# Kernel optimization log

Hardware: AMD Instinct MI355X
Metric: run time of the kernel (lower is better)

Reference implementation:

```python
import jax, jax.numpy as jnp
import numpy as np

B, T, H, HY, E, L = 32, 256, 1024, 256, 64, 2


def setup_inputs() -> dict:
    key = jax.random.key(0)
    ks = jax.random.split(key, 16)
    rn = lambda k, s, sc=0.05: jax.random.normal(k, s, dtype=jnp.float32) * sc
    return {
        'input': rn(ks[0], (B, T, H), 1.0),
        'w_ih': rn(ks[1], (L, 4 * H, H)),
        'w_hh': rn(ks[2], (L, 4 * H, H)),
        'hyper_w_ih': rn(ks[3], (L, 4 * HY, 2 * H)),
        'hyper_w_hh': rn(ks[4], (L, 4 * HY, HY)),
        'hyper_b': rn(ks[5], (L, 4 * HY)),
        'w_zh': rn(ks[6], (L, 4 * E, HY)),
        'b_zh': jnp.ones((L, 4 * E), jnp.float32),
        'w_zx': rn(ks[7], (L, 4 * E, HY)),
        'b_zx': jnp.ones((L, 4 * E), jnp.float32),
        'w_zb': rn(ks[8], (L, 4 * E, HY)),
        'w_dh': rn(ks[9], (L, 4, H, E), 1.0 / E),
        'w_dx': rn(ks[10], (L, 4, H, E), 1.0 / E),
        'w_db': rn(ks[11], (L, 4, H, E)),
        'b0': rn(ks[12], (L, 4 * H)),
    }


def reference(input, w_ih, w_hh, hyper_w_ih, hyper_w_hh, hyper_b,
              w_zh, b_zh, w_zx, b_zx, w_zb, w_dh, w_dx, w_db, b0):
    L = w_ih.shape[0]
    Bb = input.shape[0]
    Hh = w_hh.shape[-1]
    Hy = hyper_w_hh.shape[-1]
    Ee = w_dh.shape[-1]

    def cell(l, xt, h, c, hh, hc):
        # hyper (meta) LSTM step: input is concat(x, h_main)
        xh = jnp.concatenate([xt, h], axis=-1)
        hg = xh @ hyper_w_ih[l].T + hh @ hyper_w_hh[l].T + hyper_b[l]
        hi, hf, hgc, ho = jnp.split(hg, 4, axis=-1)
        hc2 = jax.nn.sigmoid(hf) * hc + jax.nn.sigmoid(hi) * jnp.tanh(hgc)
        hh2 = jax.nn.sigmoid(ho) * jnp.tanh(hc2)
        # gate-wise embeddings z (B, 4, E) then project to per-gate scale vectors (B, 4H)
        zh = (hh2 @ w_zh[l].T + b_zh[l]).reshape(Bb, 4, Ee)
        zx = (hh2 @ w_zx[l].T + b_zx[l]).reshape(Bb, 4, Ee)
        zb = (hh2 @ w_zb[l].T).reshape(Bb, 4, Ee)
        dh = jnp.einsum('bge,ghe->bgh', zh, w_dh[l]).reshape(Bb, 4 * Hh)
        dx = jnp.einsum('bge,ghe->bgh', zx, w_dx[l]).reshape(Bb, 4 * Hh)
        db = jnp.einsum('bge,ghe->bgh', zb, w_db[l]).reshape(Bb, 4 * Hh) + b0[l]
        # main LSTM gates, dynamically scaled by hypernetwork
        pre = dh * (h @ w_hh[l].T) + dx * (xt @ w_ih[l].T) + db
        i, f, g, o = jnp.split(pre, 4, axis=-1)
        c2 = jax.nn.sigmoid(f) * c + jax.nn.sigmoid(i) * jnp.tanh(g)
        h2 = jax.nn.sigmoid(o) * jnp.tanh(c2)
        return h2, c2, hh2, hc2

    def step(carry, xt):
        h, c, hh, hc = carry  # each (L, B, .)
        hs, cs, hhs, hcs = [], [], [], []
        inp = xt
        for l in range(L):
            h2, c2, hh2, hc2 = cell(l, inp, h[l], c[l], hh[l], hc[l])
            inp = h2
            hs.append(h2); cs.append(c2); hhs.append(hh2); hcs.append(hc2)
        carry = (jnp.stack(hs), jnp.stack(cs), jnp.stack(hhs), jnp.stack(hcs))
        return carry, inp  # top-layer hidden

    init = (jnp.zeros((L, Bb, Hh), input.dtype), jnp.zeros((L, Bb, Hh), input.dtype),
            jnp.zeros((L, Bb, Hy), input.dtype), jnp.zeros((L, Bb, Hy), input.dtype))
    carry, ys = jax.lax.scan(step, init, jnp.swapaxes(input, 0, 1))
    h_seq = jnp.swapaxes(ys, 0, 1)  # (B, T, H)
    return h_seq, carry[0][-1], carry[1][-1]
```

## Files before the change

kernel.cpp:

```cpp
#include <hip/hip_runtime.h>

typedef __bf16 bf16;
typedef __bf16 bf16x8 __attribute__((ext_vector_type(8)));
typedef __bf16 bf16x4 __attribute__((ext_vector_type(4)));
typedef float f32x4 __attribute__((ext_vector_type(4)));
typedef unsigned long long u64;

#define SCOPE_AGENT __HIP_MEMORY_SCOPE_AGENT


__device__ __forceinline__ float sigf(float x) { return 1.0f / (1.0f + __expf(-x)); }
__device__ __forceinline__ float tanhf_fast(float x) {
  float e = __expf(-2.0f * fabsf(x));
  float r = (1.0f - e) / (1.0f + e);
  return copysignf(r, x);
}
__device__ __forceinline__ f32x4 mfma16(bf16x8 a, bf16x8 b, f32x4 c) {
  return __builtin_amdgcn_mfma_f32_16x16x32_bf16(a, b, c, 0, 0, 0);
}
__device__ __forceinline__ u64 uld(const u64* p) { return __hip_atomic_load(p, __ATOMIC_RELAXED, SCOPE_AGENT); }
__device__ __forceinline__ void ust(u64* p, u64 v) { __hip_atomic_store(p, v, __ATOMIC_RELAXED, SCOPE_AGENT); }
__device__ __forceinline__ int ildi(const int* p) { return __hip_atomic_load(p, __ATOMIC_RELAXED, SCOPE_AGENT); }
__device__ __forceinline__ void isti(int* p, int v) { __hip_atomic_store(p, v, __ATOMIC_RELAXED, SCOPE_AGENT); }
__device__ __forceinline__ void fstf(float* p, float v) { __hip_atomic_store(p, v, __ATOMIC_RELAXED, SCOPE_AGENT); }
__device__ __forceinline__ void usti32(unsigned* p, unsigned v) { __hip_atomic_store(p, v, __ATOMIC_RELAXED, SCOPE_AGENT); }

__global__ void detect_kernel(const void* probe, int* flag) {
  __shared__ int cnt;
  if (threadIdx.x == 0) cnt = 0;
  __syncthreads();
  const bf16* p = (const bf16*)probe;
  int local = 0;
  for (int j = threadIdx.x; j < 8192; j += 256) {
    float x = (float)p[j];
    bool wild = (x != x) || (fabsf(x) > 1e3f) || (x != 0.0f && fabsf(x) < 1e-30f);
    local += wild ? 1 : 0;
  }
  atomicAdd(&cnt, local);
  __syncthreads();
  if (threadIdx.x == 0) *flag = (cnt > 64) ? 1 : 0;
}

struct CvtSrc { const void* s[15]; };
struct CvtDst { bf16* d[15]; };

__global__ __launch_bounds__(256) void convert_kernel(CvtSrc S, CvtDst D, const int* flag) {
  const int pre[16] = {0, 8388608, 16777216, 25165824, 29360128, 29884416, 29886464,
                       30017536, 30018048, 30149120, 30149632, 30280704, 30804992,
                       31329280, 31853568, 31861760};
  const int fp32 = *flag;
  const int nvec = 31861760 / 4;
  for (int v = blockIdx.x * 256 + threadIdx.x; v < nvec; v += gridDim.x * 256) {
    int e = v * 4;
    int seg = 0;
#pragma unroll
    for (int k = 1; k < 15; ++k) seg += (e >= pre[k]) ? 1 : 0;
    int off = e - pre[seg];
    bf16* d = D.d[seg] + off;
    if (fp32) {
      const float* s = (const float*)S.s[seg] + off;
      float4 x = *(const float4*)s;
      d[0] = (bf16)x.x; d[1] = (bf16)x.y; d[2] = (bf16)x.z; d[3] = (bf16)x.w;
    } else {
      const bf16* s = (const bf16*)S.s[seg] + off;
      d[0] = s[0]; d[1] = s[1]; d[2] = s[2]; d[3] = s[3];
    }
  }
}

__global__ void init_kernel(u64* zbase) {
  int i = blockIdx.x * 256 + threadIdx.x;
  zbase[i] = 0ull;
}

__global__ __launch_bounds__(256) void gemm_pre(
    const bf16* __restrict__ A, const bf16* __restrict__ w_ih_l,
    const bf16* __restrict__ hwih_l, bf16* __restrict__ Xp, float* __restrict__ Hxp) {
  constexpr int LDT = 72;
  __shared__ alignas(16) bf16 As[64 * LDT];
  __shared__ alignas(16) bf16 Bs[64 * LDT];
  const int bm = blockIdx.x & 127;
  const int bn = blockIdx.x >> 7;
  const int m0 = bm * 64, n0 = bn * 64;
  const int tid = threadIdx.x;
  const int lane = tid & 63, wid = tid >> 6;
  const int l15 = lane & 15, q = lane >> 4;
  const int srow = tid >> 2, sk = (tid & 3) * 16;
  const bf16* arow = A + (size_t)(m0 + srow) * 1024;
  const int n = n0 + srow;
  const bf16* brow = (n < 4096) ? (w_ih_l + (size_t)n * 1024)
                                : (hwih_l + (size_t)(n - 4096) * 2048);
  f32x4 acc[4] = {};
  for (int kb = 0; kb < 1024; kb += 64) {
    *(bf16x8*)(&As[srow * LDT + sk])     = *(const bf16x8*)(arow + kb + sk);
    *(bf16x8*)(&As[srow * LDT + sk + 8]) = *(const bf16x8*)(arow + kb + sk + 8);
    *(bf16x8*)(&Bs[srow * LDT + sk])     = *(const bf16x8*)(brow + kb + sk);
    *(bf16x8*)(&Bs[srow * LDT + sk + 8]) = *(const bf16x8*)(brow + kb + sk + 8);
    __syncthreads();
#pragma unroll
    for (int kk = 0; kk < 64; kk += 32) {
      bf16x8 av = *(const bf16x8*)(&As[(wid * 16 + l15) * LDT + kk + q * 8]);
#pragma unroll
      for (int j = 0; j < 4; ++j) {
        bf16x8 bv = *(const bf16x8*)(&Bs[(j * 16 + l15) * LDT + kk + q * 8]);
        acc[j] = mfma16(av, bv, acc[j]);
      }
    }
    __syncthreads();
  }
#pragma unroll
  for (int j = 0; j < 4; ++j) {
    const int gn = n0 + j * 16 + l15;
#pragma unroll
    for (int r = 0; r < 4; ++r) {
      const int gm = m0 + wid * 16 + q * 4 + r;
      float v = acc[j][r];
      if (gn < 4096) Xp[(size_t)gm * 4096 + gn] = (bf16)v;
      else           Hxp[(size_t)gm * 1024 + (gn - 4096)] = v;
    }
  }
}

struct SeqArgs {
  const bf16 *w_hh, *hwih, *hwhh, *hyb;
  const bf16 *w_zh, *b_zh, *w_zx, *b_zx, *w_zb;
  const bf16 *w_dh, *w_dx, *w_db, *b0;
  const bf16 *Xp; const float *Hxp;
  const bf16 *w_ih1;
  bf16 *Xp1c; float *Hxp1c;
  u64 *Y0;
  u64 *hpub;
  u64 *hh2pub;
  float *outp;
  int *flags;
};

__global__ __launch_bounds__(256) void seq_kernel(SeqArgs a) {
  __shared__ char smem[41472] __attribute__((aligned(16)));
  bf16 (*hstage)[1032] = (bf16(*)[1032])smem;
  bf16 (*hhK)[264]    = (bf16(*)[264])(smem + 33024);
  float* hgL          = (float*)(smem + 33024);
  bf16 (*hA4)[1032]   = (bf16(*)[1032])smem;
  bf16 (*hh2A)[264]   = (bf16(*)[264])(smem + 8256);
  float (*RhL)[256]   = (float(*)[256])(smem + 10368);
  float (*zsL)[768]   = (float(*)[768])(smem + 14464);
  float (*presL)[256] = (float(*)[256])(smem + 26752);
  bf16 (*hbuf)[64]    = (bf16(*)[64])(smem + 30848);
  bf16*  As = (bf16*)smem;
  bf16*  Bs = (bf16*)(smem + 9216);
  float* Ct = (float*)(smem + 18432);

  const int tid = threadIdx.x;
  const int lane = tid & 63, wid = tid >> 6;
  const int l15 = lane & 15, q = lane >> 4;
  const int blk = blockIdx.x;
  const int xcd = blk & 7, slot = blk >> 3;
  const int layer = xcd >> 2, xl = xcd & 3;
  const int s16 = xl * 4 + (slot & 3);
  const int bq = slot >> 2;
  const int lblk = bq * 16 + s16;
  const int hd = s16 >> 1;
  const int mh = (bq == hd) ? 0 : ((bq == ((hd + 4) & 7)) ? 1 : -1);
  const bool isHyper = (((s16 & 1) == 0) && (mh >= 0));

  u64* hbase  = a.hpub + (size_t)layer * 16384;
  u64* h2base = a.hh2pub + (size_t)layer * 4096;
  int* genp0  = a.flags;
  int* genp   = a.flags + layer * 16;
  int* gchunkp= a.flags + 32;
  int* arrp   = a.flags + 64 + layer * 2048;
  int* hh2fp  = a.flags + 4160 + layer * 256;
  int* carrp  = a.flags + 4672;

  const bf16* whh_l = a.w_hh + (size_t)layer * 4194304;
  const bf16* hybl  = a.hyb + layer * 1024;
  const bf16* bzh_l = a.b_zh + layer * 256;
  const bf16* bzx_l = a.b_zx + layer * 256;
  const bf16* b0_l  = a.b0 + (size_t)layer * 4096;
  const int cb = tid >> 6, chl = tid & 63;

  float c_reg = 0.0f;
  float hc[2] = {0, 0};

  const bf16* zrow[12];
#pragma unroll
  for (int j = 0; j < 12; ++j) {
    int ng = wid * 12 + j, tau = ng >> 4;
    const bf16* base = (tau == 0) ? a.w_zh : (tau == 1) ? a.w_zx : a.w_zb;
    zrow[j] = base + ((size_t)layer * 256 + (ng & 15) * 16 + l15) * 256;
  }
  const bf16* rrow[4];
#pragma unroll
  for (int nt = 0; nt < 4; ++nt)
    rrow[nt] = whh_l + (size_t)(wid * 1024 + s16 * 64 + nt * 16 + l15) * 1024;
  const bf16* hirow[2];
  const bf16* hhrow[2];
#pragma unroll
  for (int nt = 0; nt < 2; ++nt) {
    const int row = wid * 256 + hd * 32 + nt * 16 + l15;
    hirow[nt] = a.hwih + (size_t)layer * 2097152 + (size_t)row * 2048 + 1024;
    hhrow[nt] = a.hwhh + (size_t)layer * 262144 + (size_t)row * 256;
  }
  const size_t wdo = ((size_t)(layer * 4 + wid) * 1024 + s16 * 64 + lane) * 64;
  const bf16 *pdh = a.w_dh + wdo, *pdx = a.w_dx + wdo, *pdb = a.w_db + wdo;

  for (int t = 0; t < 256; ++t) {
    const int tloc = t & 31;
    u64* wslot = hbase + (size_t)(t & 1) * 8192;
    const u64* rslot = hbase + (size_t)((t + 1) & 1) * 8192;
    u64* wcur = h2base + (size_t)(t & 1) * 2048;
    const u64* rK = h2base + (size_t)((t + 1) & 1) * 2048;

    if (layer == 1 && tloc == 0) {
      const int k = t >> 5;
      if (tid == 0) { while (ildi(genp0) < (k + 1) * 32) __builtin_amdgcn_s_sleep(2); }
      __atomic_signal_fence(__ATOMIC_SEQ_CST);
      __syncthreads();
      const int srow = tid >> 2, sk = (tid & 3) * 16;
      for (int tt = 0; tt < 10; ++tt) {
        const int tile = lblk * 10 + tt;
        const int m0 = (tile & 15) * 64, n0 = (tile >> 4) * 64;
        const int m = m0 + srow;
        const u64* arow = a.Y0 + (((size_t)(m >> 5) * 256 + k * 32 + (m & 31)) << 8);
        const int n = n0 + srow;
        const bf16* brow = (n < 4096) ? (a.w_ih1 + (size_t)n * 1024)
                                      : (a.hwih + 2097152 + (size_t)(n - 4096) * 2048);
        f32x4 acc[4] = {};
        for (int kb = 0; kb < 1024; kb += 64) {
          const int c0 = (kb + sk) >> 2;
          u64 a0 = uld(arow + c0),     a1 = uld(arow + c0 + 1);
          u64 a2 = uld(arow + c0 + 2), a3 = uld(arow + c0 + 3);
          *(u64*)&As[srow * 72 + sk]      = a0;
          *(u64*)&As[srow * 72 + sk + 4]  = a1;
          *(u64*)&As[srow * 72 + sk + 8]  = a2;
          *(u64*)&As[srow * 72 + sk + 12] = a3;
          *(bf16x8*)&Bs[srow * 72 + sk]     = *(const bf16x8*)(brow + kb + sk);
          *(bf16x8*)&Bs[srow * 72 + sk + 8] = *(const bf16x8*)(brow + kb + sk + 8);
          __syncthreads();
#pragma unroll
          for (int kk = 0; kk < 64; kk += 32) {
            bf16x8 av = *(const bf16x8*)&As[(wid * 16 + l15) * 72 + kk + q * 8];
#pragma unroll
            for (int j = 0; j < 4; ++j) {
              bf16x8 bv = *(const bf16x8*)&Bs[(j * 16 + l15) * 72 + kk + q * 8];
              acc[j] = mfma16(av, bv, acc[j]);
            }
          }
          __syncthreads();
        }
#pragma unroll
        for (int j = 0; j < 4; ++j)
#pragma unroll
          for (int r = 0; r < 4; ++r)
            Ct[(wid * 16 + q * 4 + r) * 64 + j * 16 + l15] = acc[j][r];
        __syncthreads();
#pragma unroll
        for (int e = 0; e < 4; ++e) {
          const int qd = tid * 4 + e;
          const int row = qd >> 4, col4 = (qd & 15) * 4;
          f32x4 v = *(const f32x4*)&Ct[row * 64 + col4];
          const int gm = m0 + row, gn = n0 + col4;
          if (gn < 4096) {
            union { bf16 h[4]; u64 u; } pk;
#pragma unroll
            for (int x = 0; x < 4; ++x) pk.h[x] = (bf16)v[x];
            ust((u64*)a.Xp1c + ((((size_t)gm << 12) + gn) >> 2), pk.u);
          } else {
            float* hp = a.Hxp1c + ((size_t)gm << 10) + (gn - 4096);
#pragma unroll
            for (int x = 0; x < 4; ++x) fstf(hp + x, v[x]);
          }
        }
        __syncthreads();
      }
      __atomic_signal_fence(__ATOMIC_SEQ_CST);
      __builtin_amdgcn_s_waitcnt(0);
      __syncthreads();
      if (tid == 0) isti(carrp + lblk * 16, k + 1);
      if (lblk == 0 && wid == 0) {
        for (;;) {
          int v0 = ildi(carrp + lane * 32);
          int v1 = ildi(carrp + lane * 32 + 16);
          if (__all((v0 >= k + 1) && (v1 >= k + 1))) break;
          __builtin_amdgcn_s_sleep(2);
        }
        __atomic_signal_fence(__ATOMIC_SEQ_CST);
        if (lane == 0) isti(gchunkp, k + 1);
      }
      if (tid == 0) { while (ildi(gchunkp) < k + 1) __builtin_amdgcn_s_sleep(2); }
      __atomic_signal_fence(__ATOMIC_SEQ_CST);
      __syncthreads();
    }

    if (t > 0 && tid == 0) {
      while (ildi(genp) < t) __builtin_amdgcn_s_sleep(2);
    }
    __atomic_signal_fence(__ATOMIC_SEQ_CST);
    __syncthreads();

    if (isHyper) {
      for (int i = tid; i < 4096; i += 256) {
        int b = i >> 8, u = i & 255;
        *(u64*)&hstage[b][u * 4] = uld(rslot + ((size_t)(mh * 16 + b) << 8) + u);
      }
      for (int i = tid; i < 1024; i += 256) {
        int b = i >> 6, u = i & 63;
        *(u64*)&hhK[b][u * 4] = uld(rK + ((size_t)(mh * 16 + b) << 6) + u);
      }
      __syncthreads();
      f32x4 acc[2] = {};
      for (int kk = 0; kk < 1024; kk += 32) {
        int ko = kk + q * 8;
        bf16x8 a0 = *(const bf16x8*)&hstage[l15][ko];
#pragma unroll
        for (int nt = 0; nt < 2; ++nt) {
          bf16x8 bv = *(const bf16x8*)(hirow[nt] + ko);
          acc[nt] = mfma16(a0, bv, acc[nt]);
        }
      }
      for (int kk = 0; kk < 256; kk += 32) {
        int ko = kk + q * 8;
        bf16x8 a0 = *(const bf16x8*)&hhK[l15][ko];
#pragma unroll
        for (int nt = 0; nt < 2; ++nt) {
          bf16x8 bv = *(const bf16x8*)(hhrow[nt] + ko);
          acc[nt] = mfma16(a0, bv, acc[nt]);
        }
      }
      __syncthreads();
#pragma unroll
      for (int nt = 0; nt < 2; ++nt)
#pragma unroll
        for (int r = 0; r < 4; ++r)
          hgL[(wid * 16 + q * 4 + r) * 32 + nt * 16 + l15] = acc[nt][r];
      __syncthreads();
      {
        const int b16 = tid >> 4, d0 = (tid & 15) * 2;
        const int b = mh * 16 + b16;
        float hx2[4][2];
        if (layer == 0) {
          const float* hx = a.Hxp + ((size_t)b * 256 + t) * 1024 + hd * 32 + d0;
#pragma unroll
          for (int g = 0; g < 4; ++g) {
            hx2[g][0] = hx[g * 256]; hx2[g][1] = hx[g * 256 + 1];
          }
        } else {
          const u64* hx1 = (const u64*)a.Hxp1c + (((size_t)b * 32 + tloc) << 9)
                         + ((hd * 32 + d0) >> 1);
#pragma unroll
          for (int g = 0; g < 4; ++g) {
            u64 w = uld(hx1 + g * 128);
            hx2[g][0] = __uint_as_float((unsigned)(w & 0xffffffffu));
            hx2[g][1] = __uint_as_float((unsigned)(w >> 32));
          }
        }
        union { bf16 h[2]; unsigned u; } pk;
#pragma unroll
        for (int dd = 0; dd < 2; ++dd) {
          int d = d0 + dd, gd = hd * 32 + d;
          float hi  = hgL[(0 * 16 + b16) * 32 + d] + (float)hybl[gd]       + hx2[0][dd];
          float hf  = hgL[(1 * 16 + b16) * 32 + d] + (float)hybl[256 + gd] + hx2[1][dd];
          float hgv = hgL[(2 * 16 + b16) * 32 + d] + (float)hybl[512 + gd] + hx2[2][dd];
          float ho  = hgL[(3 * 16 + b16) * 32 + d] + (float)hybl[768 + gd] + hx2[3][dd];
          hc[dd] = sigf(hf) * hc[dd] + sigf(hi) * tanhf_fast(hgv);
          pk.h[dd] = (bf16)(sigf(ho) * tanhf_fast(hc[dd]));
        }
        usti32((unsigned*)wcur + b * 128 + hd * 16 + (d0 >> 1), pk.u);
      }
      __atomic_signal_fence(__ATOMIC_SEQ_CST);
      __builtin_amdgcn_s_waitcnt(0);
      __syncthreads();
      if (tid == 0) isti(hh2fp + (hd * 2 + mh) * 16, t + 1);
    }
    __syncthreads();

    for (int i = tid; i < 1024; i += 256) {
      int b = i >> 8, u = i & 255;
      *(u64*)&hA4[b][u * 4] = uld(rslot + ((size_t)(bq * 4 + b) << 8) + u);
    }
    __syncthreads();
    {
      f32x4 racc[4] = {};
      for (int kk = 0; kk < 1024; kk += 32) {
        const int ko = kk + q * 8;
        bf16x8 av = *(const bf16x8*)&hA4[l15 & 3][ko];
#pragma unroll
        for (int nt = 0; nt < 4; ++nt) {
          bf16x8 bv = *(const bf16x8*)(rrow[nt] + ko);
          racc[nt] = mfma16(av, bv, racc[nt]);
        }
      }
      if (lane < 16) {
#pragma unroll
        for (int nt = 0; nt < 4; ++nt)
#pragma unroll
          for (int r = 0; r < 4; ++r)
            RhL[r][wid * 64 + nt * 16 + lane] = racc[nt][r];
      }
    }
    if (tid < 16) { while (ildi(hh2fp + tid * 16) < t + 1) __builtin_amdgcn_s_sleep(1); }
    __atomic_signal_fence(__ATOMIC_SEQ_CST);
    __syncthreads();
    {
      int b = tid >> 6, u = tid & 63;
      *(u64*)&hh2A[b][u * 4] = uld(wcur + ((size_t)(bq * 4 + b) << 6) + u);
    }
    __syncthreads();
    {
      f32x4 zacc[12] = {};
      for (int kk = 0; kk < 256; kk += 32) {
        const int ko = kk + q * 8;
        bf16x8 av = *(const bf16x8*)&hh2A[l15 & 3][ko];
#pragma unroll
        for (int j = 0; j < 12; ++j) {
          bf16x8 bv = *(const bf16x8*)(zrow[j] + ko);
          zacc[j] = mfma16(av, bv, zacc[j]);
        }
      }
      if (lane < 16) {
#pragma unroll
        for (int j = 0; j < 12; ++j) {
          int ng = wid * 12 + j, tau = ng >> 4, col = (ng & 15) * 16 + lane;
          float bias = (tau == 0) ? (float)bzh_l[col] : (tau == 1) ? (float)bzx_l[col] : 0.0f;
#pragma unroll
          for (int r = 0; r < 4; ++r) zsL[r][tau * 256 + col] = zacc[j][r] + bias;
        }
      }
    }
    __syncthreads();
    {
      float dH[4] = {}, dX[4] = {}, dB[4] = {};
      for (int e0 = 0; e0 < 64; e0 += 4) {
        bf16x4 wh = *(const bf16x4*)(pdh + e0);
        bf16x4 wx = *(const bf16x4*)(pdx + e0);
        bf16x4 wb = *(const bf16x4*)(pdb + e0);
        f32x4 zh_[4], zx_[4], zb_[4];
#pragma unroll
        for (int b = 0; b < 4; ++b) {
          zh_[b] = *(const f32x4*)&zsL[b][wid * 64 + e0];
          zx_[b] = *(const f32x4*)&zsL[b][256 + wid * 64 + e0];
          zb_[b] = *(const f32x4*)&zsL[b][512 + wid * 64 + e0];
        }
#pragma unroll
        for (int jj = 0; jj < 4; ++jj) {
          float whf = (float)wh[jj], wxf = (float)wx[jj], wbf = (float)wb[jj];
#pragma unroll
          for (int b = 0; b < 4; ++b) {
            dH[b] += zh_[b][jj] * whf;
            dX[b] += zx_[b][jj] * wxf;
            dB[b] += zb_[b][jj] * wbf;
          }
        }
      }
      const int n = wid * 1024 + s16 * 64 + lane;
#pragma unroll
      for (int b = 0; b < 4; ++b) {
        float rh = RhL[b][wid * 64 + lane];
        float xp;
        if (layer == 0) {
          xp = (float)a.Xp[((size_t)(bq * 4 + b) * 256 + t) * 4096 + n];
        } else {
          u64 w = uld((const u64*)a.Xp1c
                      + ((((size_t)((bq * 4 + b) * 32 + tloc) << 12) + (n & ~3)) >> 2));
          xp = __uint_as_float(((unsigned)(w >> ((n & 3) * 16)) & 0xffffu) << 16);
        }
        float b0v = (float)b0_l[n];
        presL[b][wid * 64 + lane] = dH[b] * rh + dX[b] * xp + dB[b] + b0v;
      }
    }
    __syncthreads();
    {
      float iv = presL[cb][chl];
      float fv = presL[cb][64 + chl];
      float gv = presL[cb][128 + chl];
      float ov = presL[cb][192 + chl];
      c_reg = sigf(fv) * c_reg + sigf(iv) * tanhf_fast(gv);
      float hn = sigf(ov) * tanhf_fast(c_reg);
      hbuf[cb][chl] = (bf16)hn;
      if (layer) {
        const size_t oo = ((size_t)(bq * 4 + cb) * 256 + t) * 1024 + s16 * 64 + chl;
        a.outp[oo] = hn;
        if (t == 255) {
          a.outp[8388608 + (bq * 4 + cb) * 1024 + s16 * 64 + chl] = hn;
          a.outp[8421376 + (bq * 4 + cb) * 1024 + s16 * 64 + chl] = c_reg;
        }
      }
    }
    __syncthreads();
    if (tid < 64) {
      int b = tid >> 4, u = tid & 15;
      u64 pk = *(const u64*)&hbuf[b][u * 4];
      ust(wslot + ((size_t)(bq * 4 + b) << 8) + s16 * 16 + u, pk);
      if (layer == 0)
        ust(a.Y0 + (((size_t)(bq * 4 + b) * 256 + t) << 8) + s16 * 16 + u, pk);
    }
    __atomic_signal_fence(__ATOMIC_SEQ_CST);
    __builtin_amdgcn_s_waitcnt(0);
    __syncthreads();
    if (tid == 0) isti(arrp + lblk * 16, t + 1);
    if (lblk == 0 && wid == 0) {
      const int t1 = t + 1;
      for (;;) {
        int v0 = ildi(arrp + lane * 32);
        int v1 = ildi(arrp + lane * 32 + 16);
        if (__all((v0 >= t1) && (v1 >= t1))) break;
        __builtin_amdgcn_s_sleep(2);
      }
      __atomic_signal_fence(__ATOMIC_SEQ_CST);
      if (lane == 0) isti(genp, t1);
    }
  }
}

extern "C" void kernel_launch(void* const* d_in, const int* in_sizes, int n_in,
                              void* d_out, int out_size, void* d_ws, size_t ws_size,
                              hipStream_t stream) {
  float* outp = (float*)d_out;
  char* ws = (char*)d_ws;
  bf16*  Xp     = (bf16*) (ws);
  float* Hxp    = (float*)(ws + 67108864ull);
  u64*   Y0     = (u64*)  (ws + 100663296ull);
  bf16* c_input = (bf16*)(ws + 117669888ull);
  bf16*  Xp1c   = c_input;
  float* Hxp1c  = (float*)(ws + 117669888ull + 8388608ull);
  bf16* c_w_ih  = (bf16*)(ws + 134447104ull);
  bf16* c_w_hh  = (bf16*)(ws + 151224320ull);
  bf16* c_hwih  = (bf16*)(ws + 168001536ull);
  bf16* c_hwhh  = (bf16*)(ws + 176390144ull);
  bf16* c_hyb   = (bf16*)(ws + 177438720ull);
  bf16* c_wzh   = (bf16*)(ws + 177442816ull);
  bf16* c_bzh   = (bf16*)(ws + 177704960ull);
  bf16* c_wzx   = (bf16*)(ws + 177705984ull);
  bf16* c_bzx   = (bf16*)(ws + 177968128ull);
  bf16* c_wzb   = (bf16*)(ws + 177969152ull);
  bf16* c_wdh   = (bf16*)(ws + 178231296ull);
  bf16* c_wdx   = (bf16*)(ws + 179279872ull);
  bf16* c_wdb   = (bf16*)(ws + 180328448ull);
  bf16* c_b0    = (bf16*)(ws + 181377024ull);
  int*  dflag   = (int*) (ws + 181393408ull);
  char* pubb    = ws + 181397504ull;
  u64*   hpub   = (u64*)  (pubb + 0);
  u64*   hh2pub = (u64*)  (pubb + 262144);
  int*   flags  = (int*)  (pubb + 327680);

  hipLaunchKernelGGL(detect_kernel, dim3(1), dim3(256), 0, stream, d_in[2], dflag);
  CvtSrc S; CvtDst D;
  for (int i = 0; i < 15; ++i) S.s[i] = d_in[i];
  D.d[0] = c_input; D.d[1] = c_w_ih; D.d[2] = c_w_hh; D.d[3] = c_hwih; D.d[4] = c_hwhh;
  D.d[5] = c_hyb;   D.d[6] = c_wzh;  D.d[7] = c_bzh;  D.d[8] = c_wzx;  D.d[9] = c_bzx;
  D.d[10] = c_wzb;  D.d[11] = c_wdh; D.d[12] = c_wdx; D.d[13] = c_wdb; D.d[14] = c_b0;
  hipLaunchKernelGGL(convert_kernel, dim3(2048), dim3(256), 0, stream, S, D, dflag);

  hipLaunchKernelGGL(init_kernel, dim3(176), dim3(256), 0, stream, (u64*)pubb);
  hipLaunchKernelGGL(gemm_pre, dim3(10240), dim3(256), 0, stream,
                     c_input, c_w_ih, c_hwih, Xp, Hxp);

  SeqArgs sa;
  sa.w_hh = c_w_hh; sa.hwih = c_hwih; sa.hwhh = c_hwhh; sa.hyb = c_hyb;
  sa.w_zh = c_wzh; sa.b_zh = c_bzh; sa.w_zx = c_wzx; sa.b_zx = c_bzx; sa.w_zb = c_wzb;
  sa.w_dh = c_wdh; sa.w_dx = c_wdx; sa.w_db = c_wdb; sa.b0 = c_b0;
  sa.Xp = Xp; sa.Hxp = Hxp;
  sa.w_ih1 = c_w_ih + (size_t)4194304;
  sa.Xp1c = Xp1c; sa.Hxp1c = Hxp1c;
  sa.Y0 = Y0;
  sa.hpub = hpub; sa.hh2pub = hh2pub;
  sa.outp = outp;
  sa.flags = flags;
  hipLaunchKernelGGL(seq_kernel, dim3(256), dim3(256), 0, stream, sa);
}
```

Before: 19.70 ms.

## Replace global per-step barrier with targeted per-block dependency flag waits

```diff
diff --git a/kernel.cpp b/kernel.cpp
--- a/kernel.cpp
+++ b/kernel.cpp
@@ -162,13 +162,13 @@
   const int hd = s16 >> 1;
   const int mh = (bq == hd) ? 0 : ((bq == ((hd + 4) & 7)) ? 1 : -1);
   const bool isHyper = (((s16 & 1) == 0) && (mh >= 0));
+  const int myMh = bq >> 2;
 
   u64* hbase  = a.hpub + (size_t)layer * 16384;
   u64* h2base = a.hh2pub + (size_t)layer * 4096;
-  int* genp0  = a.flags;
-  int* genp   = a.flags + layer * 16;
   int* gchunkp= a.flags + 32;
   int* arrp   = a.flags + 64 + layer * 2048;
+  int* arrp0  = a.flags + 64;
   int* hh2fp  = a.flags + 4160 + layer * 256;
   int* carrp  = a.flags + 4672;
 
@@ -213,7 +213,11 @@
 
     if (layer == 1 && tloc == 0) {
       const int k = t >> 5;
-      if (tid == 0) { while (ildi(genp0) < (k + 1) * 32) __builtin_amdgcn_s_sleep(2); }
+      if (tid < 128) {
+        while (ildi(arrp0 + tid * 16) < (k + 1) * 32) __builtin_amdgcn_s_sleep(2);
+      } else if (t > 0) {
+        while (ildi(arrp + (tid - 128) * 16) < t) __builtin_amdgcn_s_sleep(2);
+      }
       __atomic_signal_fence(__ATOMIC_SEQ_CST);
       __syncthreads();
       const int srow = tid >> 2, sk = (tid & 3) * 16;
@@ -292,8 +296,20 @@
       __syncthreads();
     }
 
-    if (t > 0 && tid == 0) {
-      while (ildi(genp) < t) __builtin_amdgcn_s_sleep(2);
+    if (t > 0) {
+      if (tid < 16) {
+        while (ildi(arrp + (bq * 16 + tid) * 16) < t) __builtin_amdgcn_s_sleep(1);
+      }
+      if (isHyper) {
+        if (tid >= 64 && tid < 128) {
+          const int j = tid - 64;
+          const int fl = (mh * 4 + (j >> 4)) * 16 + (j & 15);
+          while (ildi(arrp + fl * 16) < t) __builtin_amdgcn_s_sleep(1);
+        }
+        if (tid >= 128 && tid < 136) {
+          while (ildi(hh2fp + ((tid - 128) * 2 + mh) * 16) < t) __builtin_amdgcn_s_sleep(1);
+        }
+      }
     }
     __atomic_signal_fence(__ATOMIC_SEQ_CST);
     __syncthreads();
@@ -398,7 +414,9 @@
             RhL[r][wid * 64 + nt * 16 + lane] = racc[nt][r];
       }
     }
-    if (tid < 16) { while (ildi(hh2fp + tid * 16) < t + 1) __builtin_amdgcn_s_sleep(1); }
+    if (tid < 8) {
+      while (ildi(hh2fp + (tid * 2 + myMh) * 16) < t + 1) __builtin_amdgcn_s_sleep(1);
+    }
     __atomic_signal_fence(__ATOMIC_SEQ_CST);
     __syncthreads();
     {
@@ -498,17 +516,6 @@
     __builtin_amdgcn_s_waitcnt(0);
     __syncthreads();
     if (tid == 0) isti(arrp + lblk * 16, t + 1);
-    if (lblk == 0 && wid == 0) {
-      const int t1 = t + 1;
-      for (;;) {
-        int v0 = ildi(arrp + lane * 32);
-        int v1 = ildi(arrp + lane * 32 + 16);
-        if (__all((v0 >= t1) && (v1 >= t1))) break;
-        __builtin_amdgcn_s_sleep(2);
-      }
-      __atomic_signal_fence(__ATOMIC_SEQ_CST);
-      if (lane == 0) isti(genp, t1);
-    }
   }
 }
 
```

New measurement: 20.41 ms. +3.6%, slower.

## Precombine hyper embedding and projection weights into direct hh2-to-gate matrices

Applied to the files above, without the earlier changes.

```diff
diff --git a/kernel.cpp b/kernel.cpp
--- a/kernel.cpp
+++ b/kernel.cpp
@@ -121,10 +121,79 @@
   }
 }
 
+__global__ __launch_bounds__(256) void wcomb_kernel(
+    const bf16* __restrict__ wzh, const bf16* __restrict__ wzx, const bf16* __restrict__ wzb,
+    const bf16* __restrict__ wdh, const bf16* __restrict__ wdx, const bf16* __restrict__ wdb,
+    bf16* __restrict__ Wc) {
+  __shared__ alignas(16) bf16 As[64 * 72];
+  __shared__ alignas(16) bf16 Bt[64 * 72];
+  const int id = blockIdx.x;
+  const int tile = id & 63, g = (id >> 6) & 3, l = (id >> 8) & 1, tau = id >> 9;
+  const int m0 = (tile >> 2) * 64, k0 = (tile & 3) * 64;
+  const bf16* wz = (tau == 0) ? wzh : (tau == 1) ? wzx : wzb;
+  const bf16* wd = (tau == 0) ? wdh : (tau == 1) ? wdx : wdb;
+  const int tid = threadIdx.x;
+  const int lane = tid & 63, wid = tid >> 6;
+  const int l15 = lane & 15, q = lane >> 4;
+  {
+    const int srow = tid >> 2, sk = (tid & 3) * 16;
+    const bf16* src = wd + ((size_t)((l * 4 + g) * 1024 + m0 + srow)) * 64 + sk;
+    *(bf16x8*)&As[srow * 72 + sk]     = *(const bf16x8*)(src);
+    *(bf16x8*)&As[srow * 72 + sk + 8] = *(const bf16x8*)(src + 8);
+  }
+  {
+    const int e = tid >> 2, kc = (tid & 3) * 16;
+    const bf16* src = wz + ((size_t)(l * 256 + g * 64 + e)) * 256 + k0 + kc;
+    bf16 v[16];
+    *(bf16x8*)v       = *(const bf16x8*)(src);
+    *(bf16x8*)(v + 8) = *(const bf16x8*)(src + 8);
+#pragma unroll
+    for (int i = 0; i < 16; ++i) Bt[(kc + i) * 72 + e] = v[i];
+  }
+  __syncthreads();
+  f32x4 acc[4] = {};
+#pragma unroll
+  for (int kk = 0; kk < 64; kk += 32) {
+    const int ko = kk + q * 8;
+    bf16x8 av = *(const bf16x8*)&As[(wid * 16 + l15) * 72 + ko];
+#pragma unroll
+    for (int j = 0; j < 4; ++j) {
+      bf16x8 bv = *(const bf16x8*)&Bt[(j * 16 + l15) * 72 + ko];
+      acc[j] = mfma16(av, bv, acc[j]);
+    }
+  }
+#pragma unroll
+  for (int j = 0; j < 4; ++j) {
+    const int gn = k0 + j * 16 + l15;
+#pragma unroll
+    for (int r = 0; r < 4; ++r) {
+      const int gm = m0 + wid * 16 + q * 4 + r;
+      Wc[(((size_t)(tau * 2 + l) * 4 + g) * 1024 + gm) * 256 + gn] = (bf16)acc[j][r];
+    }
+  }
+}
+
+__global__ void dbias_kernel(const bf16* __restrict__ bzh, const bf16* __restrict__ bzx,
+                             const bf16* __restrict__ wdh, const bf16* __restrict__ wdx,
+                             float* __restrict__ out) {
+  const int idx = blockIdx.x * 256 + threadIdx.x;
+  const int tp = idx >> 13;
+  const int rem = idx & 8191;
+  const int l = rem >> 12, row = rem & 4095;
+  const int g = row >> 10;
+  const bf16* bz = (tp ? bzx : bzh) + l * 256 + g * 64;
+  const bf16* wd = (tp ? wdx : wdh) + (size_t)(l * 4096 + row) * 64;
+  float s = 0.0f;
+#pragma unroll 8
+  for (int e = 0; e < 64; ++e) s += (float)bz[e] * (float)wd[e];
+  out[tp * 8192 + l * 4096 + row] = s;
+}
+
 struct SeqArgs {
   const bf16 *w_hh, *hwih, *hwhh, *hyb;
-  const bf16 *w_zh, *b_zh, *w_zx, *b_zx, *w_zb;
-  const bf16 *w_dh, *w_dx, *w_db, *b0;
+  const bf16 *Wc;
+  const float *dbH, *dbX;
+  const bf16 *b0;
   const bf16 *Xp; const float *Hxp;
   const bf16 *w_ih1;
   bf16 *Xp1c; float *Hxp1c;
@@ -142,10 +211,8 @@
   float* hgL          = (float*)(smem + 33024);
   bf16 (*hA4)[1032]   = (bf16(*)[1032])smem;
   bf16 (*hh2A)[264]   = (bf16(*)[264])(smem + 8256);
-  float (*RhL)[256]   = (float(*)[256])(smem + 10368);
-  float (*zsL)[768]   = (float(*)[768])(smem + 14464);
-  float (*presL)[256] = (float(*)[256])(smem + 26752);
-  bf16 (*hbuf)[64]    = (bf16(*)[64])(smem + 30848);
+  float (*presL)[256] = (float(*)[256])(smem + 10368);
+  bf16 (*hbuf)[64]    = (bf16(*)[64])(smem + 14464);
   bf16*  As = (bf16*)smem;
   bf16*  Bs = (bf16*)(smem + 9216);
   float* Ct = (float*)(smem + 18432);
@@ -174,25 +241,20 @@
 
   const bf16* whh_l = a.w_hh + (size_t)layer * 4194304;
   const bf16* hybl  = a.hyb + layer * 1024;
-  const bf16* bzh_l = a.b_zh + layer * 256;
-  const bf16* bzx_l = a.b_zx + layer * 256;
   const bf16* b0_l  = a.b0 + (size_t)layer * 4096;
   const int cb = tid >> 6, chl = tid & 63;
 
   float c_reg = 0.0f;
   float hc[2] = {0, 0};
 
-  const bf16* zrow[12];
-#pragma unroll
-  for (int j = 0; j < 12; ++j) {
-    int ng = wid * 12 + j, tau = ng >> 4;
-    const bf16* base = (tau == 0) ? a.w_zh : (tau == 1) ? a.w_zx : a.w_zb;
-    zrow[j] = base + ((size_t)layer * 256 + (ng & 15) * 16 + l15) * 256;
-  }
   const bf16* rrow[4];
 #pragma unroll
   for (int nt = 0; nt < 4; ++nt)
     rrow[nt] = whh_l + (size_t)(wid * 1024 + s16 * 64 + nt * 16 + l15) * 1024;
+  const bf16* wc0 = a.Wc + (((size_t)(0 * 2 + layer) * 4 + wid) * 1024
+                            + s16 * 64 + l15) * 256;
+  const bf16* wc1 = wc0 + (size_t)2097152;
+  const bf16* wc2 = wc1 + (size_t)2097152;
   const bf16* hirow[2];
   const bf16* hhrow[2];
 #pragma unroll
@@ -201,8 +263,6 @@
     hirow[nt] = a.hwih + (size_t)layer * 2097152 + (size_t)row * 2048 + 1024;
     hhrow[nt] = a.hwhh + (size_t)layer * 262144 + (size_t)row * 256;
   }
-  const size_t wdo = ((size_t)(layer * 4 + wid) * 1024 + s16 * 64 + lane) * 64;
-  const bf16 *pdh = a.w_dh + wdo, *pdx = a.w_dx + wdo, *pdb = a.w_db + wdo;
 
   for (int t = 0; t < 256; ++t) {
     const int tloc = t & 31;
@@ -214,6 +274,7 @@
     if (layer == 1 && tloc == 0) {
       const int k = t >> 5;
       if (tid == 0) { while (ildi(genp0) < (k + 1) * 32) __builtin_amdgcn_s_sleep(2); }
+      if (t > 0 && tid == 32) { while (ildi(genp) < t) __builtin_amdgcn_s_sleep(2); }
       __atomic_signal_fence(__ATOMIC_SEQ_CST);
       __syncthreads();
       const int srow = tid >> 2, sk = (tid & 3) * 16;
@@ -379,8 +440,8 @@
       *(u64*)&hA4[b][u * 4] = uld(rslot + ((size_t)(bq * 4 + b) << 8) + u);
     }
     __syncthreads();
+    f32x4 racc[4] = {};
     {
-      f32x4 racc[4] = {};
       for (int kk = 0; kk < 1024; kk += 32) {
         const int ko = kk + q * 8;
         bf16x8 av = *(const bf16x8*)&hA4[l15 & 3][ko];
@@ -390,13 +451,6 @@
           racc[nt] = mfma16(av, bv, racc[nt]);
         }
       }
-      if (lane < 16) {
-#pragma unroll
-        for (int nt = 0; nt < 4; ++nt)
-#pragma unroll
-          for (int r = 0; r < 4; ++r)
-            RhL[r][wid * 64 + nt * 16 + lane] = racc[nt][r];
-      }
     }
     if (tid < 16) { while (ildi(hh2fp + tid * 16) < t + 1) __builtin_amdgcn_s_sleep(1); }
     __atomic_signal_fence(__ATOMIC_SEQ_CST);
@@ -407,65 +461,40 @@
     }
     __syncthreads();
     {
-      f32x4 zacc[12] = {};
+      f32x4 dacc[12] = {};
       for (int kk = 0; kk < 256; kk += 32) {
         const int ko = kk + q * 8;
         bf16x8 av = *(const bf16x8*)&hh2A[l15 & 3][ko];
 #pragma unroll
         for (int j = 0; j < 12; ++j) {
-          bf16x8 bv = *(const bf16x8*)(zrow[j] + ko);
-          zacc[j] = mfma16(av, bv, zacc[j]);
+          const bf16* base = ((j >> 2) == 0 ? wc0 : (j >> 2) == 1 ? wc1 : wc2)
+                           + (j & 3) * 4096 + ko;
+          dacc[j] = mfma16(av, *(const bf16x8*)base, dacc[j]);
         }
       }
       if (lane < 16) {
 #pragma unroll
-        for (int j = 0; j < 12; ++j) {
-          int ng = wid * 12 + j, tau = ng >> 4, col = (ng & 15) * 16 + lane;
-          float bias = (tau == 0) ? (float)bzh_l[col] : (tau == 1) ? (float)bzx_l[col] : 0.0f;
-#pragma unroll
-          for (int r = 0; r < 4; ++r) zsL[r][tau * 256 + col] = zacc[j][r] + bias;
-        }
-      }
-    }
-    __syncthreads();
-    {
-      float dH[4] = {}, dX[4] = {}, dB[4] = {};
-      for (int e0 = 0; e0 < 64; e0 += 4) {
-        bf16x4 wh = *(const bf16x4*)(pdh + e0);
-        bf16x4 wx = *(const bf16x4*)(pdx + e0);
-        bf16x4 wb = *(const bf16x4*)(pdb + e0);
-        f32x4 zh_[4], zx_[4], zb_[4];
-#pragma unroll
-        for (int b = 0; b < 4; ++b) {
-          zh_[b] = *(const f32x4*)&zsL[b][wid * 64 + e0];
-          zx_[b] = *(const f32x4*)&zsL[b][256 + wid * 64 + e0];
-          zb_[b] = *(const f32x4*)&zsL[b][512 + wid * 64 + e0];
-        }
-#pragma unroll
-        for (int jj = 0; jj < 4; ++jj) {
-          float whf = (float)wh[jj], wxf = (float)wx[jj], wbf = (float)wb[jj];
-#pragma unroll
-          for (int b = 0; b < 4; ++b) {
-            dH[b] += zh_[b][jj] * whf;
-            dX[b] += zx_[b][jj] * wxf;
-            dB[b] += zb_[b][jj] * wbf;
+        for (int nt = 0; nt < 4; ++nt) {
+          const int row = wid * 1024 + s16 * 64 + nt * 16 + lane;
+          const float dbh = a.dbH[layer * 4096 + row];
+          const float dbx = a.dbX[layer * 4096 + row];
+          const float b0v = (float)b0_l[row];
+#pragma unroll
+          for (int r = 0; r < 4; ++r) {
+            float rh = racc[nt][r];
+            float xp;
+            if (layer == 0) {
+              xp = (float)a.Xp[((size_t)(bq * 4 + r) * 256 + t) * 4096 + row];
+            } else {
+              u64 w = uld((const u64*)a.Xp1c
+                          + ((((size_t)((bq * 4 + r) * 32 + tloc) << 12) + (row & ~3)) >> 2));
+              xp = __uint_as_float(((unsigned)(w >> ((row & 3) * 16)) & 0xffffu) << 16);
+            }
+            presL[r][wid * 64 + nt * 16 + lane] =
+                (dacc[nt][r] + dbh) * rh + (dacc[4 + nt][r] + dbx) * xp
+                + dacc[8 + nt][r] + b0v;
           }
         }
-      }
-      const int n = wid * 1024 + s16 * 64 + lane;
-#pragma unroll
-      for (int b = 0; b < 4; ++b) {
-        float rh = RhL[b][wid * 64 + lane];
-        float xp;
-        if (layer == 0) {
-          xp = (float)a.Xp[((size_t)(bq * 4 + b) * 256 + t) * 4096 + n];
-        } else {
-          u64 w = uld((const u64*)a.Xp1c
-                      + ((((size_t)((bq * 4 + b) * 32 + tloc) << 12) + (n & ~3)) >> 2));
-          xp = __uint_as_float(((unsigned)(w >> ((n & 3) * 16)) & 0xffffu) << 16);
-        }
-        float b0v = (float)b0_l[n];
-        presL[b][wid * 64 + lane] = dH[b] * rh + dX[b] * xp + dB[b] + b0v;
       }
     }
     __syncthreads();
@@ -542,6 +571,8 @@
   u64*   hpub   = (u64*)  (pubb + 0);
   u64*   hh2pub = (u64*)  (pubb + 262144);
   int*   flags  = (int*)  (pubb + 327680);
+  bf16*  Wc     = (bf16*) (ws + 181757952ull);
+  float* dbias  = (float*)(ws + 194340864ull);
 
   hipLaunchKernelGGL(detect_kernel, dim3(1), dim3(256), 0, stream, d_in[2], dflag);
   CvtSrc S; CvtDst D;
@@ -554,11 +585,15 @@
   hipLaunchKernelGGL(init_kernel, dim3(176), dim3(256), 0, stream, (u64*)pubb);
   hipLaunchKernelGGL(gemm_pre, dim3(10240), dim3(256), 0, stream,
                      c_input, c_w_ih, c_hwih, Xp, Hxp);
+  hipLaunchKernelGGL(wcomb_kernel, dim3(1536), dim3(256), 0, stream,
+                     c_wzh, c_wzx, c_wzb, c_wdh, c_wdx, c_wdb, Wc);
+  hipLaunchKernelGGL(dbias_kernel, dim3(64), dim3(256), 0, stream,
+                     c_bzh, c_bzx, c_wdh, c_wdx, dbias);
 
   SeqArgs sa;
   sa.w_hh = c_w_hh; sa.hwih = c_hwih; sa.hwhh = c_hwhh; sa.hyb = c_hyb;
-  sa.w_zh = c_wzh; sa.b_zh = c_bzh; sa.w_zx = c_wzx; sa.b_zx = c_bzx; sa.w_zb = c_wzb;
-  sa.w_dh = c_wdh; sa.w_dx = c_wdx; sa.w_db = c_wdb; sa.b0 = c_b0;
+  sa.Wc = Wc; sa.dbH = dbias; sa.dbX = dbias + 8192;
+  sa.b0 = c_b0;
   sa.Xp = Xp; sa.Hxp = Hxp;
   sa.w_ih1 = c_w_ih + (size_t)4194304;
   sa.Xp1c = Xp1c; sa.Hxp1c = Hxp1c;
```

After: 20.47 ms. 3.9% more time.

## Split each persistent block's hidden slice in half across twice as many blocks

Applied to the files above, without the earlier changes.

```diff
diff --git a/kernel.cpp b/kernel.cpp
--- a/kernel.cpp
+++ b/kernel.cpp
@@ -135,17 +135,17 @@
   int *flags;
 };
 
-__global__ __launch_bounds__(256) void seq_kernel(SeqArgs a) {
+__global__ __launch_bounds__(256, 2) void seq_kernel(SeqArgs a) {
   __shared__ char smem[41472] __attribute__((aligned(16)));
   bf16 (*hstage)[1032] = (bf16(*)[1032])smem;
   bf16 (*hhK)[264]    = (bf16(*)[264])(smem + 33024);
   float* hgL          = (float*)(smem + 33024);
   bf16 (*hA4)[1032]   = (bf16(*)[1032])smem;
   bf16 (*hh2A)[264]   = (bf16(*)[264])(smem + 8256);
-  float (*RhL)[256]   = (float(*)[256])(smem + 10368);
-  float (*zsL)[768]   = (float(*)[768])(smem + 14464);
-  float (*presL)[256] = (float(*)[256])(smem + 26752);
-  bf16 (*hbuf)[64]    = (bf16(*)[64])(smem + 30848);
+  float (*RhL)[128]   = (float(*)[128])(smem + 10368);
+  float (*zsL)[768]   = (float(*)[768])(smem + 12416);
+  float (*presL)[128] = (float(*)[128])(smem + 24704);
+  bf16 (*hbuf)[32]    = (bf16(*)[32])(smem + 26752);
   bf16*  As = (bf16*)smem;
   bf16*  Bs = (bf16*)(smem + 9216);
   float* Ct = (float*)(smem + 18432);
@@ -154,30 +154,30 @@
   const int lane = tid & 63, wid = tid >> 6;
   const int l15 = lane & 15, q = lane >> 4;
   const int blk = blockIdx.x;
-  const int xcd = blk & 7, slot = blk >> 3;
+  const int xcd = blk & 7, slot2 = blk >> 3;
   const int layer = xcd >> 2, xl = xcd & 3;
-  const int s16 = xl * 4 + (slot & 3);
-  const int bq = slot >> 2;
-  const int lblk = bq * 16 + s16;
+  const int half = slot2 & 1, slot = slot2 >> 1;
+  const int bq = slot >> 2, sq = slot & 3;
+  const int s16 = sq * 4 + xl;
+  const int lblk2 = (bq * 16 + s16) * 2 + half;
   const int hd = s16 >> 1;
   const int mh = (bq == hd) ? 0 : ((bq == ((hd + 4) & 7)) ? 1 : -1);
-  const bool isHyper = (((s16 & 1) == 0) && (mh >= 0));
+  const bool isHyper = (((s16 & 1) == 0) && (mh >= 0) && (half == 0));
 
   u64* hbase  = a.hpub + (size_t)layer * 16384;
   u64* h2base = a.hh2pub + (size_t)layer * 4096;
   int* genp0  = a.flags;
   int* genp   = a.flags + layer * 16;
   int* gchunkp= a.flags + 32;
-  int* arrp   = a.flags + 64 + layer * 2048;
-  int* hh2fp  = a.flags + 4160 + layer * 256;
-  int* carrp  = a.flags + 4672;
+  int* arrp   = a.flags + 64 + layer * 4096;
+  int* hh2fp  = a.flags + 8256 + layer * 256;
+  int* carrp  = a.flags + 8768;
 
   const bf16* whh_l = a.w_hh + (size_t)layer * 4194304;
   const bf16* hybl  = a.hyb + layer * 1024;
   const bf16* bzh_l = a.b_zh + layer * 256;
   const bf16* bzx_l = a.b_zx + layer * 256;
   const bf16* b0_l  = a.b0 + (size_t)layer * 4096;
-  const int cb = tid >> 6, chl = tid & 63;
 
   float c_reg = 0.0f;
   float hc[2] = {0, 0};
@@ -189,10 +189,10 @@
     const bf16* base = (tau == 0) ? a.w_zh : (tau == 1) ? a.w_zx : a.w_zb;
     zrow[j] = base + ((size_t)layer * 256 + (ng & 15) * 16 + l15) * 256;
   }
-  const bf16* rrow[4];
-#pragma unroll
-  for (int nt = 0; nt < 4; ++nt)
-    rrow[nt] = whh_l + (size_t)(wid * 1024 + s16 * 64 + nt * 16 + l15) * 1024;
+  const bf16* rrow[2];
+#pragma unroll
+  for (int nt = 0; nt < 2; ++nt)
+    rrow[nt] = whh_l + (size_t)(wid * 1024 + s16 * 64 + half * 32 + nt * 16 + l15) * 1024;
   const bf16* hirow[2];
   const bf16* hhrow[2];
 #pragma unroll
@@ -201,7 +201,8 @@
     hirow[nt] = a.hwih + (size_t)layer * 2097152 + (size_t)row * 2048 + 1024;
     hhrow[nt] = a.hwhh + (size_t)layer * 262144 + (size_t)row * 256;
   }
-  const size_t wdo = ((size_t)(layer * 4 + wid) * 1024 + s16 * 64 + lane) * 64;
+  const size_t wdo = ((size_t)(layer * 4 + wid) * 1024 + s16 * 64 + half * 32
+                      + (lane & 31)) * 64;
   const bf16 *pdh = a.w_dh + wdo, *pdx = a.w_dx + wdo, *pdb = a.w_db + wdo;
 
   for (int t = 0; t < 256; ++t) {
@@ -214,11 +215,12 @@
     if (layer == 1 && tloc == 0) {
       const int k = t >> 5;
       if (tid == 0) { while (ildi(genp0) < (k + 1) * 32) __builtin_amdgcn_s_sleep(2); }
+      if (t > 0 && tid == 32) { while (ildi(genp) < t) __builtin_amdgcn_s_sleep(2); }
       __atomic_signal_fence(__ATOMIC_SEQ_CST);
       __syncthreads();
       const int srow = tid >> 2, sk = (tid & 3) * 16;
-      for (int tt = 0; tt < 10; ++tt) {
-        const int tile = lblk * 10 + tt;
+      for (int tt = 0; tt < 5; ++tt) {
+        const int tile = lblk2 * 5 + tt;
         const int m0 = (tile & 15) * 64, n0 = (tile >> 4) * 64;
         const int m = m0 + srow;
         const u64* arow = a.Y0 + (((size_t)(m >> 5) * 256 + k * 32 + (m & 31)) << 8);
@@ -276,12 +278,14 @@
       __atomic_signal_fence(__ATOMIC_SEQ_CST);
       __builtin_amdgcn_s_waitcnt(0);
       __syncthreads();
-      if (tid == 0) isti(carrp + lblk * 16, k + 1);
-      if (lblk == 0 && wid == 0) {
+      if (tid == 0) isti(carrp + lblk2 * 16, k + 1);
+      if (lblk2 == 0 && wid == 0) {
         for (;;) {
-          int v0 = ildi(carrp + lane * 32);
-          int v1 = ildi(carrp + lane * 32 + 16);
-          if (__all((v0 >= k + 1) && (v1 >= k + 1))) break;
+          int v0 = ildi(carrp + lane * 64);
+          int v1 = ildi(carrp + lane * 64 + 16);
+          int v2 = ildi(carrp + lane * 64 + 32);
+          int v3 = ildi(carrp + lane * 64 + 48);
+          if (__all((v0 >= k + 1) && (v1 >= k + 1) && (v2 >= k + 1) && (v3 >= k + 1))) break;
           __builtin_amdgcn_s_sleep(2);
         }
         __atomic_signal_fence(__ATOMIC_SEQ_CST);
@@ -380,22 +384,22 @@
     }
     __syncthreads();
     {
-      f32x4 racc[4] = {};
+      f32x4 racc[2] = {};
       for (int kk = 0; kk < 1024; kk += 32) {
         const int ko = kk + q * 8;
         bf16x8 av = *(const bf16x8*)&hA4[l15 & 3][ko];
 #pragma unroll
-        for (int nt = 0; nt < 4; ++nt) {
+        for (int nt = 0; nt < 2; ++nt) {
           bf16x8 bv = *(const bf16x8*)(rrow[nt] + ko);
           racc[nt] = mfma16(av, bv, racc[nt]);
         }
       }
       if (lane < 16) {
 #pragma unroll
-        for (int nt = 0; nt < 4; ++nt)
+        for (int nt = 0; nt < 2; ++nt)
 #pragma unroll
           for (int r = 0; r < 4; ++r)
-            RhL[r][wid * 64 + nt * 16 + lane] = racc[nt][r];
+            RhL[r][wid * 32 + nt * 16 + lane] = racc[nt][r];
       }
     }
     if (tid < 16) { while (ildi(hh2fp + tid * 16) < t + 1) __builtin_amdgcn_s_sleep(1); }
@@ -428,7 +432,7 @@
       }
     }
     __syncthreads();
-    {
+    if (lane < 32) {
       float dH[4] = {}, dX[4] = {}, dB[4] = {};
       for (int e0 = 0; e0 < 64; e0 += 4) {
         bf16x4 wh = *(const bf16x4*)(pdh + e0);
@@ -452,10 +456,10 @@
           }
         }
       }
-      const int n = wid * 1024 + s16 * 64 + lane;
+      const int n = wid * 1024 + s16 * 64 + half * 32 + lane;
 #pragma unroll
       for (int b = 0; b < 4; ++b) {
-        float rh = RhL[b][wid * 64 + lane];
+        float rh = RhL[b][wid * 32 + lane];
         float xp;
         if (layer == 0) {
           xp = (float)a.Xp[((size_t)(bq * 4 + b) * 256 + t) * 4096 + n];
@@ -465,45 +469,49 @@
           xp = __uint_as_float(((unsigned)(w >> ((n & 3) * 16)) & 0xffffu) << 16);
         }
         float b0v = (float)b0_l[n];
-        presL[b][wid * 64 + lane] = dH[b] * rh + dX[b] * xp + dB[b] + b0v;
-      }
-    }
-    __syncthreads();
-    {
+        presL[b][wid * 32 + lane] = dH[b] * rh + dX[b] * xp + dB[b] + b0v;
+      }
+    }
+    __syncthreads();
+    if (tid < 128) {
+      const int cb = tid >> 5, chl = tid & 31;
       float iv = presL[cb][chl];
-      float fv = presL[cb][64 + chl];
-      float gv = presL[cb][128 + chl];
-      float ov = presL[cb][192 + chl];
+      float fv = presL[cb][32 + chl];
+      float gv = presL[cb][64 + chl];
+      float ov = presL[cb][96 + chl];
       c_reg = sigf(fv) * c_reg + sigf(iv) * tanhf_fast(gv);
       float hn = sigf(ov) * tanhf_fast(c_reg);
       hbuf[cb][chl] = (bf16)hn;
       if (layer) {
-        const size_t oo = ((size_t)(bq * 4 + cb) * 256 + t) * 1024 + s16 * 64 + chl;
+        const size_t oo = ((size_t)(bq * 4 + cb) * 256 + t) * 1024
+                        + s16 * 64 + half * 32 + chl;
         a.outp[oo] = hn;
         if (t == 255) {
-          a.outp[8388608 + (bq * 4 + cb) * 1024 + s16 * 64 + chl] = hn;
-          a.outp[8421376 + (bq * 4 + cb) * 1024 + s16 * 64 + chl] = c_reg;
-        }
-      }
-    }
-    __syncthreads();
-    if (tid < 64) {
-      int b = tid >> 4, u = tid & 15;
+          a.outp[8388608 + (bq * 4 + cb) * 1024 + s16 * 64 + half * 32 + chl] = hn;
+          a.outp[8421376 + (bq * 4 + cb) * 1024 + s16 * 64 + half * 32 + chl] = c_reg;
+        }
+      }
+    }
+    __syncthreads();
+    if (tid < 32) {
+      int b = tid >> 3, u = tid & 7;
       u64 pk = *(const u64*)&hbuf[b][u * 4];
-      ust(wslot + ((size_t)(bq * 4 + b) << 8) + s16 * 16 + u, pk);
+      ust(wslot + ((size_t)(bq * 4 + b) << 8) + s16 * 16 + half * 8 + u, pk);
       if (layer == 0)
-        ust(a.Y0 + (((size_t)(bq * 4 + b) * 256 + t) << 8) + s16 * 16 + u, pk);
+        ust(a.Y0 + (((size_t)(bq * 4 + b) * 256 + t) << 8) + s16 * 16 + half * 8 + u, pk);
     }
     __atomic_signal_fence(__ATOMIC_SEQ_CST);
     __builtin_amdgcn_s_waitcnt(0);
     __syncthreads();
-    if (tid == 0) isti(arrp + lblk * 16, t + 1);
-    if (lblk == 0 && wid == 0) {
+    if (tid == 0) isti(arrp + lblk2 * 16, t + 1);
+    if (lblk2 == 0 && wid == 0) {
       const int t1 = t + 1;
       for (;;) {
-        int v0 = ildi(arrp + lane * 32);
-        int v1 = ildi(arrp + lane * 32 + 16);
-        if (__all((v0 >= t1) && (v1 >= t1))) break;
+        int v0 = ildi(arrp + lane * 64);
+        int v1 = ildi(arrp + lane * 64 + 16);
+        int v2 = ildi(arrp + lane * 64 + 32);
+        int v3 = ildi(arrp + lane * 64 + 48);
+        if (__all((v0 >= t1) && (v1 >= t1) && (v2 >= t1) && (v3 >= t1))) break;
         __builtin_amdgcn_s_sleep(2);
       }
       __atomic_signal_fence(__ATOMIC_SEQ_CST);
@@ -551,7 +559,7 @@
   D.d[10] = c_wzb;  D.d[11] = c_wdh; D.d[12] = c_wdx; D.d[13] = c_wdb; D.d[14] = c_b0;
   hipLaunchKernelGGL(convert_kernel, dim3(2048), dim3(256), 0, stream, S, D, dflag);
 
-  hipLaunchKernelGGL(init_kernel, dim3(176), dim3(256), 0, stream, (u64*)pubb);
+  hipLaunchKernelGGL(init_kernel, dim3(192), dim3(256), 0, stream, (u64*)pubb);
   hipLaunchKernelGGL(gemm_pre, dim3(10240), dim3(256), 0, stream,
                      c_input, c_w_ih, c_hwih, Xp, Hxp);
 
@@ -566,5 +574,5 @@
   sa.hpub = hpub; sa.hh2pub = hh2pub;
   sa.outp = outp;
   sa.flags = flags;
-  hipLaunchKernelGGL(seq_kernel, dim3(256), dim3(256), 0, stream, sa);
-}
+  hipLaunchKernelGGL(seq_kernel, dim3(512), dim3(256), 0, stream, sa);
+}
```

After: 23.66 ms. +20.1%, slower.
